# Optimization experiments

Measured on AMD Instinct MI355X. Metric: run time of the kernel, lower is better.

The kernel has to match this reference:

```python
import jax, jax.numpy as jnp
import numpy as np

B, S, D = 8, 2048, 512


def setup_inputs() -> dict:
    key = jax.random.key(0)
    ks = jax.random.split(key, 8)
    x = jax.random.normal(ks[0], (B, S, D), dtype=jnp.float32)
    mask = jax.random.randint(ks[1], (B, S, 1), 0, 2, dtype=jnp.int32)
    Wq = jax.random.normal(ks[2], (D, D), dtype=jnp.float32) / np.sqrt(D)
    bq = jax.random.normal(ks[3], (D,), dtype=jnp.float32) * 0.01
    Wk = jax.random.normal(ks[4], (D, D), dtype=jnp.float32) / np.sqrt(D)
    bk = jax.random.normal(ks[5], (D,), dtype=jnp.float32) * 0.01
    Wv = jax.random.normal(ks[6], (D, D), dtype=jnp.float32) / np.sqrt(D)
    bv = jax.random.normal(ks[7], (D,), dtype=jnp.float32) * 0.01
    return {"x": x, "mask": mask, "Wq": Wq, "bq": bq, "Wk": Wk, "bk": bk, "Wv": Wv, "bv": bv}


def reference(x, mask, Wq, bq, Wk, bk, Wv, bv):
    # torch Linear: y = x @ W^T + b
    Q = jnp.einsum('bsd,ed->bse', x, Wq) + bq
    K = jnp.einsum('bsd,ed->bse', x, Wk) + bk
    V = jnp.einsum('bsd,ed->bse', x, Wv) + bv
    scale = 1.0 / jnp.sqrt(jnp.asarray(x.shape[-1], dtype=x.dtype))
    scores = jnp.einsum('bqd,bkd->bqk', Q, K) * scale  # [B, S, S]
    attn_mask = jnp.transpose(mask, (0, 2, 1))  # [B, 1, S], broadcasts over queries
    scores = jnp.where(attn_mask == 0, jnp.asarray(-10000.0, dtype=scores.dtype), scores)
    attn = jax.nn.softmax(scores, axis=-1)
    return jnp.einsum('bqk,bkd->bqd', attn, V)
```

## Files before the change

kernel.cpp:

```cpp
#include <hip/hip_runtime.h>
#include <cstddef>

#define BB 8
#define SS 2048
#define DD 512
#define MM (BB * SS)

typedef __attribute__((ext_vector_type(8))) short bf16x8;
typedef __attribute__((ext_vector_type(4))) float f32x4;
typedef __attribute__((ext_vector_type(4))) unsigned short u16x4;

__device__ __forceinline__ f32x4 mfma16(bf16x8 a, bf16x8 b, f32x4 c) {
  return __builtin_amdgcn_mfma_f32_16x16x32_bf16(a, b, c, 0, 0, 0);
}
__device__ __forceinline__ unsigned short f2bf(float f) {
  unsigned int u = __float_as_uint(f);
  u += 0x7fffu + ((u >> 16) & 1u);
  return (unsigned short)(u >> 16);
}
__device__ __forceinline__ void gld16(const void* g, void* l) {
  __builtin_amdgcn_global_load_lds((const __attribute__((address_space(1))) void*)g,
                                   (__attribute__((address_space(3))) void*)l, 16, 0, 0);
}

__global__ void cvt_bf16_kernel(const float* __restrict__ in,
                                unsigned short* __restrict__ out, int n4) {
  int i = blockIdx.x * blockDim.x + threadIdx.x;
  if (i >= n4) return;
  f32x4 v = reinterpret_cast<const f32x4*>(in)[i];
  u16x4 o;
  o[0] = f2bf(v[0]);
  o[1] = f2bf(v[1]);
  o[2] = f2bf(v[2]);
  o[3] = f2bf(v[3]);
  reinterpret_cast<u16x4*>(out)[i] = o;
}

__global__ void mask_scan_kernel(const int* __restrict__ mask, int* __restrict__ idx,
                                 int* __restrict__ nbArr) {
  __shared__ int part[256];
  const int b = blockIdx.x;
  const int t = threadIdx.x;
  int m[8], c = 0;
#pragma unroll
  for (int e = 0; e < 8; ++e) {
    m[e] = mask[b * SS + t * 8 + e];
    c += (m[e] != 0);
  }
  int v = c;
  part[t] = v;
  __syncthreads();
  for (int off = 1; off < 256; off <<= 1) {
    int u = (t >= off) ? part[t - off] : 0;
    __syncthreads();
    v += u;
    part[t] = v;
    __syncthreads();
  }
  int base = v - c;
#pragma unroll
  for (int e = 0; e < 8; ++e)
    if (m[e]) idx[b * SS + base++] = t * 8 + e;
  if (t == 255) nbArr[b] = part[255];
}

__global__ void gatherk_kernel(const unsigned short* __restrict__ K,
                               const int* __restrict__ idx, const int* __restrict__ nbArr,
                               unsigned short* __restrict__ Kc) {
  const int b = blockIdx.y;
  const int j = blockIdx.x * 4 + (threadIdx.x >> 6);
  const int l = threadIdx.x & 63;
  if (j >= nbArr[b]) return;
  const int src = idx[b * SS + j];
  bf16x8 v = *reinterpret_cast<const bf16x8*>(&K[((size_t)b * SS + src) * DD + l * 8]);
  *reinterpret_cast<bf16x8*>(&Kc[((size_t)b * SS + j) * DD + l * 8]) = v;
}

__global__ __launch_bounds__(256, 2) void qkv_gemm_kernel(
    const unsigned short* __restrict__ X, const unsigned short* __restrict__ W0,
    const unsigned short* __restrict__ W1, const unsigned short* __restrict__ W2,
    const float* __restrict__ b0, const float* __restrict__ b1,
    const float* __restrict__ b2, unsigned short* __restrict__ O0,
    unsigned short* __restrict__ O1, unsigned short* __restrict__ O2) {
  __shared__ unsigned char a_lds[256 * 128];
  __shared__ unsigned char b_lds[128 * 128];
  const int tid = threadIdx.x;
  const int w = tid >> 6, l = tid & 63, lr = l & 15, hi = l >> 4;
  const int which = blockIdx.y >> 2;
  const unsigned short* W = which == 0 ? W0 : (which == 1 ? W1 : W2);
  const float* bias = which == 0 ? b0 : (which == 1 ? b1 : b2);
  unsigned short* out = which == 0 ? O0 : (which == 1 ? O1 : O2);
  const int m0 = blockIdx.x * 256;
  const int n0 = (blockIdx.y & 3) * 128;
  const int srow = l >> 3, gchunk = (l & 7) ^ (srow & 7);

  f32x4 acc[4][8];
#pragma unroll
  for (int mt = 0; mt < 4; ++mt)
#pragma unroll
    for (int nt = 0; nt < 8; ++nt) acc[mt][nt] = (f32x4){0.f, 0.f, 0.f, 0.f};

  const unsigned short* ga = X + (size_t)(m0 + w * 64 + srow) * DD + gchunk * 8;
  const unsigned short* gb = W + (size_t)(n0 + w * 32 + srow) * DD + gchunk * 8;

  for (int k0 = 0; k0 < DD; k0 += 64) {
#pragma unroll
    for (int ii = 0; ii < 8; ++ii)
      gld16(ga + (size_t)(ii * 8) * DD + k0, &a_lds[(w * 8 + ii) * 1024]);
#pragma unroll
    for (int ii = 0; ii < 4; ++ii)
      gld16(gb + (size_t)(ii * 8) * DD + k0, &b_lds[(w * 4 + ii) * 1024]);
    __syncthreads();
#pragma unroll
    for (int dkl = 0; dkl < 2; ++dkl) {
      const int gc = dkl * 4 + hi;
      bf16x8 af[4], bfr[8];
#pragma unroll
      for (int mt = 0; mt < 4; ++mt) {
        const int row = w * 64 + mt * 16 + lr;
        af[mt] = *reinterpret_cast<const bf16x8*>(
            &a_lds[row * 128 + ((gc ^ (row & 7)) * 16)]);
      }
#pragma unroll
      for (int nt = 0; nt < 8; ++nt) {
        const int row = nt * 16 + lr;
        bfr[nt] = *reinterpret_cast<const bf16x8*>(
            &b_lds[row * 128 + ((gc ^ (row & 7)) * 16)]);
      }
#pragma unroll
      for (int mt = 0; mt < 4; ++mt)
#pragma unroll
        for (int nt = 0; nt < 8; ++nt)
          acc[mt][nt] = mfma16(af[mt], bfr[nt], acc[mt][nt]);
    }
    __syncthreads();
  }

#pragma unroll
  for (int nt = 0; nt < 8; ++nt) {
    const int col = n0 + nt * 16 + lr;
    const float bv = bias[col];
#pragma unroll
    for (int mt = 0; mt < 4; ++mt)
#pragma unroll
      for (int r = 0; r < 4; ++r) {
        const int row = m0 + w * 64 + mt * 16 + hi * 4 + r;
        out[(size_t)row * DD + col] = f2bf(acc[mt][nt][r] + bv);
      }
  }
}

__global__ void vtrans_kernel(const unsigned short* __restrict__ V,
                              const int* __restrict__ idx, const int* __restrict__ nbArr,
                              unsigned short* __restrict__ VT2) {
  __shared__ unsigned short t[64][72];
  const int b = blockIdx.z;
  const int kt = blockIdx.x;
  const int d0 = blockIdx.y * 64;
  const int tid = threadIdx.x;
  const int c = tid & 63, rg = tid >> 6;
  const int nb = nbArr[b];
#pragma unroll
  for (int i = 0; i < 16; ++i) {
    const int row = rg * 16 + i;
    const int s = kt * 64 + row;
    const int src = s < nb ? idx[b * SS + s] : 0;
    t[row][c] = V[((size_t)b * SS + src) * DD + d0 + c];
  }
  __syncthreads();
#pragma unroll
  for (int i = 0; i < 16; ++i) {
    const int ix = i * 256 + tid;
    const int jj = ix & 7;
    const int dl = (ix >> 3) & 63;
    const int cc = ix >> 9;
    VT2[(((size_t)(b * 32 + kt) * 8 + cc) * 512 + d0 + dl) * 8 + jj] =
        t[cc * 8 + jj][dl];
  }
}

__global__ __launch_bounds__(256, 1) void attn_kernel(
    const unsigned short* __restrict__ Q, const unsigned short* __restrict__ Kc,
    const unsigned short* __restrict__ VT2, const int* __restrict__ nbArr,
    float* __restrict__ out) {
  __shared__ unsigned char k_lds[2][32 * 1040];
  __shared__ unsigned char vt_lds[2][4 * 512 * 16];
  __shared__ unsigned short pbuf[4][16][32];
  const int tid = threadIdx.x;
  const int w = tid >> 6, l = tid & 63, lr = l & 15, hi = l >> 4;
  const int b = blockIdx.y;
  const int q0 = blockIdx.x * 64 + w * 16;
  const float scale = 0.044194173824159216f;

  const int nb = nbArr[b];
  const int ntile = (nb + 31) >> 5;

  const unsigned short* __restrict__ Qb = Q + (size_t)b * SS * DD;
  const unsigned short* __restrict__ Kb = Kc + (size_t)b * SS * DD;
  const unsigned short* __restrict__ Vb = VT2 + (size_t)b * SS * DD;

  bf16x8 qf[16];
#pragma unroll
  for (int dk = 0; dk < 16; ++dk)
    qf[dk] = *reinterpret_cast<const bf16x8*>(
        &Qb[(size_t)(q0 + lr) * DD + dk * 32 + hi * 8]);

  f32x4 oacc[32];
#pragma unroll
  for (int i = 0; i < 32; ++i) oacc[i] = (f32x4){0.f, 0.f, 0.f, 0.f};
  float mrow[4], lrow[4];
#pragma unroll
  for (int r = 0; r < 4; ++r) {
    mrow[r] = -10000.0f;
    lrow[r] = 0.0f;
  }

  const unsigned short* kg = Kb + (size_t)(w * 8) * DD + l * 8;
  const unsigned short* vg = Vb + (size_t)(w * 512) * 8 + l * 8;

  auto stage = [&](int kt, int bufi) {
#pragma unroll
    for (int r = 0; r < 8; ++r)
      gld16(kg + (size_t)(kt * 32 + r) * DD, &k_lds[bufi][(w * 8 + r) * 1040]);
#pragma unroll
    for (int g = 0; g < 8; ++g)
      gld16(vg + ((size_t)kt * 4 * 512 + g * 64) * 8,
            &vt_lds[bufi][(w * 512 + g * 64) * 16]);
  };

  if (ntile > 0) stage(0, 0);

  for (int kt = 0; kt < ntile; ++kt) {
    __syncthreads();
    if (kt + 1 < ntile) stage(kt + 1, (kt + 1) & 1);
    const int bufi = kt & 1;

    f32x4 sacc[2];
#pragma unroll
    for (int nt = 0; nt < 2; ++nt) sacc[nt] = (f32x4){0.f, 0.f, 0.f, 0.f};
#pragma unroll
    for (int dk = 0; dk < 16; ++dk) {
#pragma unroll
      for (int nt = 0; nt < 2; ++nt) {
        bf16x8 bk = *reinterpret_cast<const bf16x8*>(
            &k_lds[bufi][(nt * 16 + lr) * 1040 + dk * 64 + hi * 16]);
        sacc[nt] = mfma16(qf[dk], bk, sacc[nt]);
      }
    }

    float s[2][4];
#pragma unroll
    for (int nt = 0; nt < 2; ++nt) {
      const int j = kt * 32 + nt * 16 + lr;
      const bool ok = j < nb;
#pragma unroll
      for (int r = 0; r < 4; ++r)
        s[nt][r] = ok ? sacc[nt][r] * scale : -10000.0f;
    }

    float mnew[4], alpha[4];
#pragma unroll
    for (int r = 0; r < 4; ++r) {
      float mx = fmaxf(s[0][r], s[1][r]);
#pragma unroll
      for (int off = 1; off < 16; off <<= 1) mx = fmaxf(mx, __shfl_xor(mx, off));
      mnew[r] = fmaxf(mrow[r], mx);
      alpha[r] = __expf(mrow[r] - mnew[r]);
      mrow[r] = mnew[r];
    }
    float rs[4] = {0.f, 0.f, 0.f, 0.f};
#pragma unroll
    for (int nt = 0; nt < 2; ++nt)
#pragma unroll
      for (int r = 0; r < 4; ++r) {
        float p = __expf(s[nt][r] - mnew[r]);
        s[nt][r] = p;
        rs[r] += p;
      }
#pragma unroll
    for (int r = 0; r < 4; ++r) {
      float t = rs[r];
#pragma unroll
      for (int off = 1; off < 16; off <<= 1) t += __shfl_xor(t, off);
      lrow[r] = lrow[r] * alpha[r] + t;
    }

#pragma unroll
    for (int nt = 0; nt < 2; ++nt)
#pragma unroll
      for (int r = 0; r < 4; ++r)
        pbuf[w][hi * 4 + r][nt * 16 + lr] = f2bf(s[nt][r]);
    bf16x8 pf = *reinterpret_cast<const bf16x8*>(&pbuf[w][lr][hi * 8]);

#pragma unroll
    for (int nt2 = 0; nt2 < 32; ++nt2) {
      f32x4 c = oacc[nt2];
#pragma unroll
      for (int r = 0; r < 4; ++r) c[r] *= alpha[r];
      bf16x8 v0 = *reinterpret_cast<const bf16x8*>(
          &vt_lds[bufi][(hi * 512 + nt2 * 16 + lr) * 16]);
      oacc[nt2] = mfma16(pf, v0, c);
    }
  }

  float inv[4];
#pragma unroll
  for (int r = 0; r < 4; ++r) inv[r] = 1.0f / lrow[r];
#pragma unroll
  for (int nt2 = 0; nt2 < 32; ++nt2)
#pragma unroll
    for (int r = 0; r < 4; ++r)
      out[((size_t)b * SS + q0 + hi * 4 + r) * DD + nt2 * 16 + lr] =
          oacc[nt2][r] * inv[r];
}

extern "C" void kernel_launch(void* const* d_in, const int* in_sizes, int n_in,
                              void* d_out, int out_size, void* d_ws, size_t ws_size,
                              hipStream_t stream) {
  const float* x = (const float*)d_in[0];
  const int* mask = (const int*)d_in[1];
  const float* Wq = (const float*)d_in[2];
  const float* bq = (const float*)d_in[3];
  const float* Wk = (const float*)d_in[4];
  const float* bk = (const float*)d_in[5];
  const float* Wv = (const float*)d_in[6];
  const float* bv = (const float*)d_in[7];
  float* out = (float*)d_out;

  char* ws = (char*)d_ws;
  const size_t MB = 1024 * 1024;
  unsigned short* Xb = (unsigned short*)(ws);
  unsigned short* Qb = (unsigned short*)(ws + 16 * MB);
  unsigned short* Kb = (unsigned short*)(ws + 32 * MB);
  unsigned short* Vb = (unsigned short*)(ws + 48 * MB);
  unsigned short* VT2b = (unsigned short*)(ws + 64 * MB);
  unsigned short* Wqb = (unsigned short*)(ws + 80 * MB);
  unsigned short* Wkb = Wqb + 512 * 512;
  unsigned short* Wvb = Wkb + 512 * 512;
  int* idx = (int*)(ws + 80 * MB + 2 * MB);
  int* nbArr = (int*)(ws + 80 * MB + 2 * MB + 65536);
  unsigned short* Kc = Xb;

  cvt_bf16_kernel<<<8192, 256, 0, stream>>>(x, Xb, (MM * DD) / 4);
  cvt_bf16_kernel<<<256, 256, 0, stream>>>(Wq, Wqb, (DD * DD) / 4);
  cvt_bf16_kernel<<<256, 256, 0, stream>>>(Wk, Wkb, (DD * DD) / 4);
  cvt_bf16_kernel<<<256, 256, 0, stream>>>(Wv, Wvb, (DD * DD) / 4);

  mask_scan_kernel<<<BB, 256, 0, stream>>>(mask, idx, nbArr);

  qkv_gemm_kernel<<<dim3(MM / 256, 12), 256, 0, stream>>>(
      Xb, Wqb, Wkb, Wvb, bq, bk, bv, Qb, Kb, Vb);

  gatherk_kernel<<<dim3(SS / 4, BB), 256, 0, stream>>>(Kb, idx, nbArr, Kc);
  vtrans_kernel<<<dim3(SS / 64, DD / 64, BB), 256, 0, stream>>>(Vb, idx, nbArr, VT2b);

  attn_kernel<<<dim3(SS / 64, BB), 256, 0, stream>>>(Qb, Kc, VT2b, nbArr, out);
}
```

Before: 276.0 us.

## Split attention keys across two blocks, gather K in-kernel, retile QKV GEMM

The attention kernel now splits each query tile's key range into two halves, each handled by a separate block. Partial outputs and the (max, sum) statistics are written out, and a new combine kernel merges them. This doubles the grid and allows two blocks per CU. The separate K-gather kernel is removed: K rows are gathered through idx directly in the attention loads, using swizzled LDS, and the mask scan zero-fills idx past nb so padded rows stay valid. Other changes: double buffering is dropped, the alpha rescale is skipped when all alphas are 1, the QKV GEMM uses 128x128 tiles with a 2x2 wave layout, and the three weight conversions are fused into one launch. The cost is an extra full-size partial-output buffer plus a combine pass, and the loss of load/compute overlap.

```diff
diff --git a/kernel.cpp b/kernel.cpp
--- a/kernel.cpp
+++ b/kernel.cpp
@@ -35,6 +35,20 @@
   o[3] = f2bf(v[3]);
   reinterpret_cast<u16x4*>(out)[i] = o;
 }
+__global__ void cvt_w3_kernel(const float* __restrict__ s0, const float* __restrict__ s1,
+                              const float* __restrict__ s2, unsigned short* __restrict__ d0,
+                              unsigned short* __restrict__ d1, unsigned short* __restrict__ d2) {
+  const float* s = blockIdx.y == 0 ? s0 : (blockIdx.y == 1 ? s1 : s2);
+  unsigned short* d = blockIdx.y == 0 ? d0 : (blockIdx.y == 1 ? d1 : d2);
+  int i = blockIdx.x * blockDim.x + threadIdx.x;
+  f32x4 v = reinterpret_cast<const f32x4*>(s)[i];
+  u16x4 o;
+  o[0] = f2bf(v[0]);
+  o[1] = f2bf(v[1]);
+  o[2] = f2bf(v[2]);
+  o[3] = f2bf(v[3]);
+  reinterpret_cast<u16x4*>(d)[i] = o;
+}
 
 __global__ void mask_scan_kernel(const int* __restrict__ mask, int* __restrict__ idx,
                                  int* __restrict__ nbArr) {
@@ -61,19 +75,9 @@
 #pragma unroll
   for (int e = 0; e < 8; ++e)
     if (m[e]) idx[b * SS + base++] = t * 8 + e;
-  if (t == 255) nbArr[b] = part[255];
-}
-
-__global__ void gatherk_kernel(const unsigned short* __restrict__ K,
-                               const int* __restrict__ idx, const int* __restrict__ nbArr,
-                               unsigned short* __restrict__ Kc) {
-  const int b = blockIdx.y;
-  const int j = blockIdx.x * 4 + (threadIdx.x >> 6);
-  const int l = threadIdx.x & 63;
-  if (j >= nbArr[b]) return;
-  const int src = idx[b * SS + j];
-  bf16x8 v = *reinterpret_cast<const bf16x8*>(&K[((size_t)b * SS + src) * DD + l * 8]);
-  *reinterpret_cast<bf16x8*>(&Kc[((size_t)b * SS + j) * DD + l * 8]) = v;
+  const int nb = part[255];
+  if (t == 255) nbArr[b] = nb;
+  for (int j = nb + t; j < SS; j += 256) idx[b * SS + j] = 0;
 }
 
 __global__ __launch_bounds__(256, 2) void qkv_gemm_kernel(
@@ -82,7 +86,7 @@
     const float* __restrict__ b0, const float* __restrict__ b1,
     const float* __restrict__ b2, unsigned short* __restrict__ O0,
     unsigned short* __restrict__ O1, unsigned short* __restrict__ O2) {
-  __shared__ unsigned char a_lds[256 * 128];
+  __shared__ unsigned char a_lds[128 * 128];
   __shared__ unsigned char b_lds[128 * 128];
   const int tid = threadIdx.x;
   const int w = tid >> 6, l = tid & 63, lr = l & 15, hi = l >> 4;
@@ -90,61 +94,61 @@
   const unsigned short* W = which == 0 ? W0 : (which == 1 ? W1 : W2);
   const float* bias = which == 0 ? b0 : (which == 1 ? b1 : b2);
   unsigned short* out = which == 0 ? O0 : (which == 1 ? O1 : O2);
-  const int m0 = blockIdx.x * 256;
+  const int m0 = blockIdx.x * 128;
   const int n0 = (blockIdx.y & 3) * 128;
+  const int wm = (w >> 1) * 64, wn = (w & 1) * 64;
   const int srow = l >> 3, gchunk = (l & 7) ^ (srow & 7);
 
-  f32x4 acc[4][8];
+  f32x4 acc[4][4];
 #pragma unroll
   for (int mt = 0; mt < 4; ++mt)
 #pragma unroll
-    for (int nt = 0; nt < 8; ++nt) acc[mt][nt] = (f32x4){0.f, 0.f, 0.f, 0.f};
-
-  const unsigned short* ga = X + (size_t)(m0 + w * 64 + srow) * DD + gchunk * 8;
+    for (int nt = 0; nt < 4; ++nt) acc[mt][nt] = (f32x4){0.f, 0.f, 0.f, 0.f};
+
+  const unsigned short* ga = X + (size_t)(m0 + w * 32 + srow) * DD + gchunk * 8;
   const unsigned short* gb = W + (size_t)(n0 + w * 32 + srow) * DD + gchunk * 8;
 
   for (int k0 = 0; k0 < DD; k0 += 64) {
 #pragma unroll
-    for (int ii = 0; ii < 8; ++ii)
-      gld16(ga + (size_t)(ii * 8) * DD + k0, &a_lds[(w * 8 + ii) * 1024]);
-#pragma unroll
-    for (int ii = 0; ii < 4; ++ii)
-      gld16(gb + (size_t)(ii * 8) * DD + k0, &b_lds[(w * 4 + ii) * 1024]);
+    for (int ii = 0; ii < 4; ++ii) {
+      gld16(ga + (size_t)ii * 8 * DD + k0, &a_lds[(w * 4 + ii) * 1024]);
+      gld16(gb + (size_t)ii * 8 * DD + k0, &b_lds[(w * 4 + ii) * 1024]);
+    }
     __syncthreads();
 #pragma unroll
     for (int dkl = 0; dkl < 2; ++dkl) {
       const int gc = dkl * 4 + hi;
-      bf16x8 af[4], bfr[8];
+      bf16x8 af[4], bfr[4];
 #pragma unroll
       for (int mt = 0; mt < 4; ++mt) {
-        const int row = w * 64 + mt * 16 + lr;
+        const int row = wm + mt * 16 + lr;
         af[mt] = *reinterpret_cast<const bf16x8*>(
             &a_lds[row * 128 + ((gc ^ (row & 7)) * 16)]);
       }
 #pragma unroll
-      for (int nt = 0; nt < 8; ++nt) {
-        const int row = nt * 16 + lr;
+      for (int nt = 0; nt < 4; ++nt) {
+        const int row = wn + nt * 16 + lr;
         bfr[nt] = *reinterpret_cast<const bf16x8*>(
             &b_lds[row * 128 + ((gc ^ (row & 7)) * 16)]);
       }
 #pragma unroll
       for (int mt = 0; mt < 4; ++mt)
 #pragma unroll
-        for (int nt = 0; nt < 8; ++nt)
+        for (int nt = 0; nt < 4; ++nt)
           acc[mt][nt] = mfma16(af[mt], bfr[nt], acc[mt][nt]);
     }
     __syncthreads();
   }
 
 #pragma unroll
-  for (int nt = 0; nt < 8; ++nt) {
-    const int col = n0 + nt * 16 + lr;
+  for (int nt = 0; nt < 4; ++nt) {
+    const int col = n0 + wn + nt * 16 + lr;
     const float bv = bias[col];
 #pragma unroll
     for (int mt = 0; mt < 4; ++mt)
 #pragma unroll
       for (int r = 0; r < 4; ++r) {
-        const int row = m0 + w * 64 + mt * 16 + hi * 4 + r;
+        const int row = m0 + wm + mt * 16 + hi * 4 + r;
         out[(size_t)row * DD + col] = f2bf(acc[mt][nt][r] + bv);
       }
   }
@@ -179,25 +183,33 @@
   }
 }
 
-__global__ __launch_bounds__(256, 1) void attn_kernel(
-    const unsigned short* __restrict__ Q, const unsigned short* __restrict__ Kc,
-    const unsigned short* __restrict__ VT2, const int* __restrict__ nbArr,
-    float* __restrict__ out) {
-  __shared__ unsigned char k_lds[2][32 * 1040];
-  __shared__ unsigned char vt_lds[2][4 * 512 * 16];
+__global__ __launch_bounds__(256, 2) void attn_kernel(
+    const unsigned short* __restrict__ Q, const unsigned short* __restrict__ K,
+    const unsigned short* __restrict__ VT2, const int* __restrict__ idx,
+    const int* __restrict__ nbArr, float* __restrict__ Out,
+    float* __restrict__ Apart, float* __restrict__ mlpart) {
+  __shared__ unsigned char k_lds[32 * 1024];
+  __shared__ unsigned char vt_lds[4 * 512 * 16];
   __shared__ unsigned short pbuf[4][16][32];
   const int tid = threadIdx.x;
   const int w = tid >> 6, l = tid & 63, lr = l & 15, hi = l >> 4;
-  const int b = blockIdx.y;
-  const int q0 = blockIdx.x * 64 + w * 16;
+  const int bid = blockIdx.x;
+  const int b = bid & 7;
+  const int qt = (bid >> 3) >> 1;
+  const int sp = (bid >> 3) & 1;
+  const int q0 = qt * 64 + w * 16;
   const float scale = 0.044194173824159216f;
 
   const int nb = nbArr[b];
   const int ntile = (nb + 31) >> 5;
+  const int half = (ntile + 1) >> 1;
+  const int lo = sp == 0 ? 0 : half;
+  const int hi_t = sp == 0 ? half : ntile;
 
   const unsigned short* __restrict__ Qb = Q + (size_t)b * SS * DD;
-  const unsigned short* __restrict__ Kb = Kc + (size_t)b * SS * DD;
+  const unsigned short* __restrict__ Kb = K + (size_t)b * SS * DD;
   const unsigned short* __restrict__ Vb = VT2 + (size_t)b * SS * DD;
+  const int* __restrict__ idxb = idx + b * SS;
 
   bf16x8 qf[16];
 #pragma unroll
@@ -215,25 +227,20 @@
     lrow[r] = 0.0f;
   }
 
-  const unsigned short* kg = Kb + (size_t)(w * 8) * DD + l * 8;
-  const unsigned short* vg = Vb + (size_t)(w * 512) * 8 + l * 8;
-
-  auto stage = [&](int kt, int bufi) {
-#pragma unroll
-    for (int r = 0; r < 8; ++r)
-      gld16(kg + (size_t)(kt * 32 + r) * DD, &k_lds[bufi][(w * 8 + r) * 1040]);
+  for (int t = lo; t < hi_t; ++t) {
+#pragma unroll
+    for (int r = 0; r < 8; ++r) {
+      const int row = w * 8 + r;
+      const int j = t * 32 + row;
+      const int src = idxb[j];
+      const int ch = (l & 56) | ((l ^ row) & 7);
+      gld16(Kb + (size_t)src * DD + ch * 8, &k_lds[row * 1024]);
+    }
+    const size_t vbase = ((size_t)((t >> 1) * 8 + (t & 1) * 4 + w) * 512);
 #pragma unroll
     for (int g = 0; g < 8; ++g)
-      gld16(vg + ((size_t)kt * 4 * 512 + g * 64) * 8,
-            &vt_lds[bufi][(w * 512 + g * 64) * 16]);
-  };
-
-  if (ntile > 0) stage(0, 0);
-
-  for (int kt = 0; kt < ntile; ++kt) {
-    __syncthreads();
-    if (kt + 1 < ntile) stage(kt + 1, (kt + 1) & 1);
-    const int bufi = kt & 1;
+      gld16(Vb + (vbase + g * 64 + l) * 8, &vt_lds[(w * 512 + g * 64) * 16]);
+    __syncthreads();
 
     f32x4 sacc[2];
 #pragma unroll
@@ -242,8 +249,10 @@
     for (int dk = 0; dk < 16; ++dk) {
 #pragma unroll
       for (int nt = 0; nt < 2; ++nt) {
+        const int row = nt * 16 + lr;
+        const int c = dk * 4 + hi;
         bf16x8 bk = *reinterpret_cast<const bf16x8*>(
-            &k_lds[bufi][(nt * 16 + lr) * 1040 + dk * 64 + hi * 16]);
+            &k_lds[row * 1024 + ((c & ~7) | ((c ^ row) & 7)) * 16]);
         sacc[nt] = mfma16(qf[dk], bk, sacc[nt]);
       }
     }
@@ -251,7 +260,7 @@
     float s[2][4];
 #pragma unroll
     for (int nt = 0; nt < 2; ++nt) {
-      const int j = kt * 32 + nt * 16 + lr;
+      const int j = t * 32 + nt * 16 + lr;
       const bool ok = j < nb;
 #pragma unroll
       for (int r = 0; r < 4; ++r)
@@ -279,10 +288,10 @@
       }
 #pragma unroll
     for (int r = 0; r < 4; ++r) {
-      float t = rs[r];
-#pragma unroll
-      for (int off = 1; off < 16; off <<= 1) t += __shfl_xor(t, off);
-      lrow[r] = lrow[r] * alpha[r] + t;
+      float tt = rs[r];
+#pragma unroll
+      for (int off = 1; off < 16; off <<= 1) tt += __shfl_xor(tt, off);
+      lrow[r] = lrow[r] * alpha[r] + tt;
     }
 
 #pragma unroll
@@ -292,26 +301,56 @@
         pbuf[w][hi * 4 + r][nt * 16 + lr] = f2bf(s[nt][r]);
     bf16x8 pf = *reinterpret_cast<const bf16x8*>(&pbuf[w][lr][hi * 8]);
 
+    const float aprod = alpha[0] * alpha[1] * alpha[2] * alpha[3];
+    unsigned long long bal = __ballot(aprod == 1.0f);
+    if (bal != ~0ull) {
+#pragma unroll
+      for (int nt2 = 0; nt2 < 32; ++nt2)
+#pragma unroll
+        for (int r = 0; r < 4; ++r) oacc[nt2][r] *= alpha[r];
+    }
 #pragma unroll
     for (int nt2 = 0; nt2 < 32; ++nt2) {
-      f32x4 c = oacc[nt2];
-#pragma unroll
-      for (int r = 0; r < 4; ++r) c[r] *= alpha[r];
       bf16x8 v0 = *reinterpret_cast<const bf16x8*>(
-          &vt_lds[bufi][(hi * 512 + nt2 * 16 + lr) * 16]);
-      oacc[nt2] = mfma16(pf, v0, c);
-    }
-  }
-
-  float inv[4];
-#pragma unroll
-  for (int r = 0; r < 4; ++r) inv[r] = 1.0f / lrow[r];
+          &vt_lds[(hi * 512 + nt2 * 16 + lr) * 16]);
+      oacc[nt2] = mfma16(pf, v0, oacc[nt2]);
+    }
+    __syncthreads();
+  }
+
+  float* Ap = sp == 0 ? Out : Apart;
 #pragma unroll
   for (int nt2 = 0; nt2 < 32; ++nt2)
 #pragma unroll
     for (int r = 0; r < 4; ++r)
-      out[((size_t)b * SS + q0 + hi * 4 + r) * DD + nt2 * 16 + lr] =
-          oacc[nt2][r] * inv[r];
+      Ap[((size_t)b * SS + q0 + hi * 4 + r) * DD + nt2 * 16 + lr] = oacc[nt2][r];
+  if (lr == 0) {
+#pragma unroll
+    for (int r = 0; r < 4; ++r) {
+      const size_t row = (size_t)sp * MM + b * SS + q0 + hi * 4 + r;
+      mlpart[row * 2 + 0] = mrow[r];
+      mlpart[row * 2 + 1] = lrow[r];
+    }
+  }
+}
+
+__global__ void combine_kernel(float* __restrict__ Out, const float* __restrict__ Apart,
+                               const float* __restrict__ mlpart) {
+  const int gid = blockIdx.x * 256 + threadIdx.x;
+  const int row = gid >> 7;
+  const float m1 = mlpart[(size_t)row * 2 + 0];
+  const float l1 = mlpart[(size_t)row * 2 + 1];
+  const float m2 = mlpart[((size_t)MM + row) * 2 + 0];
+  const float l2 = mlpart[((size_t)MM + row) * 2 + 1];
+  const float m = fmaxf(m1, m2);
+  const float w1 = __expf(m1 - m), w2 = __expf(m2 - m);
+  const float inv = 1.0f / (w1 * l1 + w2 * l2);
+  f32x4 a1 = reinterpret_cast<f32x4*>(Out)[gid];
+  f32x4 a2 = reinterpret_cast<const f32x4*>(Apart)[gid];
+  f32x4 o;
+#pragma unroll
+  for (int e = 0; e < 4; ++e) o[e] = (w1 * a1[e] + w2 * a2[e]) * inv;
+  reinterpret_cast<f32x4*>(Out)[gid] = o;
 }
 
 extern "C" void kernel_launch(void* const* d_in, const int* in_sizes, int n_in,
@@ -329,30 +368,29 @@
 
   char* ws = (char*)d_ws;
   const size_t MB = 1024 * 1024;
-  unsigned short* Xb = (unsigned short*)(ws);
-  unsigned short* Qb = (unsigned short*)(ws + 16 * MB);
-  unsigned short* Kb = (unsigned short*)(ws + 32 * MB);
-  unsigned short* Vb = (unsigned short*)(ws + 48 * MB);
-  unsigned short* VT2b = (unsigned short*)(ws + 64 * MB);
+  unsigned short* Qb = (unsigned short*)(ws);
+  unsigned short* Kb = (unsigned short*)(ws + 16 * MB);
+  unsigned short* VT2b = (unsigned short*)(ws + 32 * MB);
+  unsigned short* Xb = (unsigned short*)(ws + 48 * MB);
+  unsigned short* Vb = (unsigned short*)(ws + 64 * MB);
+  float* Apart = (float*)(ws + 48 * MB);
   unsigned short* Wqb = (unsigned short*)(ws + 80 * MB);
   unsigned short* Wkb = Wqb + 512 * 512;
   unsigned short* Wvb = Wkb + 512 * 512;
-  int* idx = (int*)(ws + 80 * MB + 2 * MB);
-  int* nbArr = (int*)(ws + 80 * MB + 2 * MB + 65536);
-  unsigned short* Kc = Xb;
+  int* idx = (int*)(ws + 82 * MB);
+  int* nbArr = (int*)(ws + 82 * MB + 65536);
+  float* mlpart = (float*)(ws + 82 * MB + 128 * 1024);
 
   cvt_bf16_kernel<<<8192, 256, 0, stream>>>(x, Xb, (MM * DD) / 4);
-  cvt_bf16_kernel<<<256, 256, 0, stream>>>(Wq, Wqb, (DD * DD) / 4);
-  cvt_bf16_kernel<<<256, 256, 0, stream>>>(Wk, Wkb, (DD * DD) / 4);
-  cvt_bf16_kernel<<<256, 256, 0, stream>>>(Wv, Wvb, (DD * DD) / 4);
-
+  cvt_w3_kernel<<<dim3(256, 3), 256, 0, stream>>>(Wq, Wk, Wv, Wqb, Wkb, Wvb);
   mask_scan_kernel<<<BB, 256, 0, stream>>>(mask, idx, nbArr);
 
-  qkv_gemm_kernel<<<dim3(MM / 256, 12), 256, 0, stream>>>(
+  qkv_gemm_kernel<<<dim3(MM / 128, 12), 256, 0, stream>>>(
       Xb, Wqb, Wkb, Wvb, bq, bk, bv, Qb, Kb, Vb);
 
-  gatherk_kernel<<<dim3(SS / 4, BB), 256, 0, stream>>>(Kb, idx, nbArr, Kc);
   vtrans_kernel<<<dim3(SS / 64, DD / 64, BB), 256, 0, stream>>>(Vb, idx, nbArr, VT2b);
 
-  attn_kernel<<<dim3(SS / 64, BB), 256, 0, stream>>>(Qb, Kc, VT2b, nbArr, out);
-}
+  attn_kernel<<<512, 256, 0, stream>>>(Qb, Kb, VT2b, idx, nbArr, out, Apart, mlpart);
+
+  combine_kernel<<<(MM * DD / 4) / 256, 256, 0, stream>>>(out, Apart, mlpart);
+}
```

Result: faster. 252.1 us (-8.7%).
